# Optimization experiments

Hardware: AMD Instinct MI355X
Metric: run time of the kernel (lower is better)

The kernel has to match this reference:

```python
import jax, jax.numpy as jnp
import numpy as np

B, L, C = 8, 4096, 256  # batches, points per batch, channels
C8 = C // 8             # query/key projection dim


def setup_inputs() -> dict:
    key = jax.random.key(0)
    ks = jax.random.split(key, 8)
    feats = jax.random.normal(ks[0], (B * L, C), dtype=jnp.float32)
    s_in = 1.0 / np.sqrt(C)
    Wq = jax.random.normal(ks[1], (C8, C), dtype=jnp.float32) * s_in
    bq = jax.random.normal(ks[2], (C8,), dtype=jnp.float32) * 0.01
    Wk = jax.random.normal(ks[3], (C8, C), dtype=jnp.float32) * s_in
    bk = jax.random.normal(ks[4], (C8,), dtype=jnp.float32) * 0.01
    Wv = jax.random.normal(ks[5], (C, C), dtype=jnp.float32) * s_in
    bv = jax.random.normal(ks[6], (C,), dtype=jnp.float32) * 0.01
    # torch init is gamma=0 which zeroes the attention branch; use a nonzero
    # scalar so the attention path contributes to output/gradients.
    gamma = jnp.float32(0.5)
    return {"feats": feats, "Wq": Wq, "bq": bq, "Wk": Wk, "bk": bk,
            "Wv": Wv, "bv": bv, "gamma": gamma,
            "batch_size": B, "points_per_batch": L}


def reference(feats, Wq, bq, Wk, bk, Wv, bv, gamma, batch_size, points_per_batch):
    n, c = feats.shape
    x = feats.reshape(batch_size, points_per_batch, c)  # [B, L, C]
    # conv1d with kernel_size=1 == per-point linear projection
    q = jnp.einsum('blc,dc->bld', x, Wq) + bq  # [B, L, C8]
    k = jnp.einsum('blc,dc->bld', x, Wk) + bk  # [B, L, C8]
    v = jnp.einsum('blc,dc->bld', x, Wv) + bv  # [B, L, C]
    energy = jnp.einsum('bid,bjd->bij', q, k)  # unscaled scores [B, L, L]
    attn = jax.nn.softmax(energy, axis=-1)
    # torch: out[c, l] = sum_j V[c, j] * attn[l, j]  -> [B, C, L]
    out_cl = jnp.einsum('bjc,blj->bcl', v, attn)
    # faithful to torch .view(batch_size, C): raw reshape of [C, L] -> [L, C]
    out = out_cl.reshape(batch_size, points_per_batch, c)
    y = gamma * out + x
    return y.reshape(n, c)
```

## Files before the change

kernel.cpp:

```cpp
#include <hip/hip_runtime.h>

#define LOG2E 1.44269504088896340736f

typedef __attribute__((ext_vector_type(4)))  float  f32x4;
typedef __attribute__((ext_vector_type(16))) float  f32x16;
typedef __attribute__((ext_vector_type(8)))  __bf16 bf16x8;
typedef __attribute__((ext_vector_type(4)))  __bf16 bf16x4;

static __device__ __forceinline__ f32x4 mfma16(bf16x8 a, bf16x8 b, f32x4 c) {
  return __builtin_amdgcn_mfma_f32_16x16x32_bf16(a, b, c, 0, 0, 0);
}
static __device__ __forceinline__ f32x16 mfma32(bf16x8 a, bf16x8 b, f32x16 c) {
  return __builtin_amdgcn_mfma_f32_32x32x16_bf16(a, b, c, 0, 0, 0);
}


__global__ void cvt_f32_to_bf16(const float* __restrict__ s, __bf16* __restrict__ d, int n4) {
  const int stride = gridDim.x * blockDim.x;
  for (int i = blockIdx.x * blockDim.x + threadIdx.x; i < n4; i += stride) {
    const float4 v = reinterpret_cast<const float4*>(s)[i];
    bf16x4 o = { (__bf16)v.x, (__bf16)v.y, (__bf16)v.z, (__bf16)v.w };
    reinterpret_cast<bf16x4*>(d)[i] = o;
  }
}

__global__ __launch_bounds__(256) void cvt_weights(
    const float* __restrict__ wq, const float* __restrict__ wk, const float* __restrict__ wv,
    __bf16* __restrict__ dq, __bf16* __restrict__ dk, __bf16* __restrict__ dv) {
  const int i = blockIdx.x * 256 + threadIdx.x;
  const float* s; __bf16* d; int off;
  if (i < 2048)      { s = wq; d = dq; off = i; }
  else if (i < 4096) { s = wk; d = dk; off = i - 2048; }
  else               { s = wv; d = dv; off = i - 4096; }
  const float4 v = reinterpret_cast<const float4*>(s)[off];
  bf16x4 o = { (__bf16)v.x, (__bf16)v.y, (__bf16)v.z, (__bf16)v.w };
  reinterpret_cast<bf16x4*>(d)[off] = o;
}

__global__ __launch_bounds__(256) void qk_proj(
    const __bf16* __restrict__ x, const __bf16* __restrict__ wq, const __bf16* __restrict__ wk,
    const float* __restrict__ bq, const float* __restrict__ bk,
    __bf16* __restrict__ Qh, __bf16* __restrict__ Ql,
    __bf16* __restrict__ Kh, __bf16* __restrict__ Kl)
{
  const int w = threadIdx.x >> 6, lane = threadIdx.x & 63;
  const int lo = lane & 15, hi = lane >> 4;
  const int m0 = blockIdx.x * 64 + w * 16;
  f32x4 acc[4] = {};
  for (int ks = 0; ks < 8; ++ks) {
    const bf16x8 a = *reinterpret_cast<const bf16x8*>(x + (size_t)(m0 + lo) * 256 + ks * 32 + hi * 8);
    #pragma unroll
    for (int nt = 0; nt < 4; ++nt) {
      const int d = nt * 16 + lo;
      const __bf16* wrow = (nt < 2) ? (wq + d * 256) : (wk + (d - 32) * 256);
      const bf16x8 bfr = *reinterpret_cast<const bf16x8*>(wrow + ks * 32 + hi * 8);
      acc[nt] = mfma16(a, bfr, acc[nt]);
    }
  }
  #pragma unroll
  for (int nt = 0; nt < 4; ++nt) {
    const int d = nt * 16 + lo;
    const float bias = (nt < 2) ? bq[d] : bk[d - 32];
    #pragma unroll
    for (int r = 0; r < 4; ++r) {
      const size_t row = m0 + hi * 4 + r;
      float v = acc[nt][r] + bias;
      if (nt < 2) v *= LOG2E;
      const __bf16 vh = (__bf16)v;
      const __bf16 vl = (__bf16)(v - (float)vh);
      if (nt < 2) { Qh[row * 32 + d] = vh;        Ql[row * 32 + d] = vl; }
      else        { Kh[row * 32 + (d - 32)] = vh; Kl[row * 32 + (d - 32)] = vl; }
    }
  }
}

__global__ __launch_bounds__(256) void v_proj(
    const __bf16* __restrict__ x, const __bf16* __restrict__ wv, const float* __restrict__ bv,
    __bf16* __restrict__ VT)
{
  const int w = threadIdx.x >> 6, lane = threadIdx.x & 63;
  const int lo = lane & 15, hi = lane >> 4;
  const int bn = blockIdx.x & 511, bc = blockIdx.x >> 9;
  const int n0 = bn * 64;
  const int c0 = bc * 64 + w * 16;
  f32x4 acc[4] = {};
  for (int ks = 0; ks < 8; ++ks) {
    const bf16x8 a = *reinterpret_cast<const bf16x8*>(wv + (size_t)(c0 + lo) * 256 + ks * 32 + hi * 8);
    #pragma unroll
    for (int nt = 0; nt < 4; ++nt) {
      const bf16x8 bfr = *reinterpret_cast<const bf16x8*>(x + (size_t)(n0 + nt * 16 + lo) * 256 + ks * 32 + hi * 8);
      acc[nt] = mfma16(bfr, a, acc[nt]);
    }
  }
  const int bb = n0 >> 12;
  const int c = c0 + lo;
  const float bias = bv[c];
  #pragma unroll
  for (int nt = 0; nt < 4; ++nt) {
    const int n = (n0 + nt * 16 + hi * 4) & 4095;
    bf16x4 pk = { (__bf16)(acc[nt][0] + bias), (__bf16)(acc[nt][1] + bias),
                  (__bf16)(acc[nt][2] + bias), (__bf16)(acc[nt][3] + bias) };
    *reinterpret_cast<bf16x4*>(VT + (size_t)(bb * 256 + c) * 4096 + n) = pk;
  }
}

__global__ __launch_bounds__(512) void attn_kernel(
    const __bf16* __restrict__ Qhi, const __bf16* __restrict__ Qlo,
    const __bf16* __restrict__ Khi, const __bf16* __restrict__ Klo,
    const __bf16* __restrict__ VT,
    const float* __restrict__ feats, const float* __restrict__ gptr,
    float* __restrict__ out)
{
  __shared__ alignas(16) __bf16 vlds[2][8][1024];
  __shared__ alignas(16) __bf16 pbuf[2][4096];

  const int tid = threadIdx.x;
  const int w   = tid >> 6, lane = tid & 63;
  const int lo  = lane & 15, hi = lane >> 4;
  const int l31 = lane & 31, h  = lane >> 5;
  const int qt  = w & 3, jt = w >> 2;
  const int b    = blockIdx.x & 7;
  const int qblk = (blockIdx.x >> 3) * 64;

  const int qi = (b * 4096 + qblk + qt * 16 + lo) * 32 + hi * 8;
  const bf16x8 qh_ = *reinterpret_cast<const bf16x8*>(Qhi + qi);
  const bf16x8 ql_ = *reinterpret_cast<const bf16x8*>(Qlo + qi);

  const int kbase = (b * 4096 + jt * 16 + lo) * 32 + hi * 8;

  const __bf16* vsrc[2];
  #pragma unroll
  for (int g = 0; g < 2; ++g) {
    const int cl = g * 16 + (lane >> 2);
    const int sl = (lane & 3) ^ ((cl >> 1) & 3);
    vsrc[g] = VT + (size_t)(b * 256 + w * 32 + cl) * 4096 + sl * 8;
  }

  const int q    = qt * 16 + lo;
  const int swq  = (q ^ (q >> 3)) & 7;
  const int pwby = q * 128 + (((jt * 2 + (hi >> 1)) ^ swq) << 4) + ((hi & 1) << 3);
  int prow[2], swp[2];
  #pragma unroll
  for (int qg = 0; qg < 2; ++qg) {
    const int qq = qg * 32 + l31;
    prow[qg] = qq * 128;
    swp[qg]  = (qq ^ (qq >> 3)) & 7;
  }
  const int vswz = (l31 >> 1) & 3;

  f32x16 o0 = {}, o1 = {};
  f32x4  lacc = {};
  bf16x8 kh[2], kl[2];

  #define STAGE_V(JB, BUF)                                                        \
    { _Pragma("unroll")                                                           \
      for (int g = 0; g < 2; ++g) {                                               \
        __builtin_amdgcn_global_load_lds(                                         \
            (const __attribute__((address_space(1))) void*)(vsrc[g] + (JB)),      \
            (__attribute__((address_space(3))) void*)(&vlds[BUF][w][g * 512 + lane * 8]), \
            16, 0, 0);                                                            \
      } }

  #define QKSM(CUR)                                                               \
    { f32x4 s_ = {0.f, 0.f, 0.f, 0.f};                                            \
      s_ = mfma16(kh[CUR], qh_, s_);                                              \
      s_ = mfma16(kl[CUR], qh_, s_);                                              \
      s_ = mfma16(kh[CUR], ql_, s_);                                              \
      f32x4 p4;                                                                   \
      _Pragma("unroll")                                                           \
      for (int r = 0; r < 4; ++r) p4[r] = __builtin_amdgcn_exp2f(s_[r]);          \
      lacc += p4;                                                                 \
      bf16x4 pk = { (__bf16)p4[0], (__bf16)p4[1], (__bf16)p4[2], (__bf16)p4[3] }; \
      *reinterpret_cast<bf16x4*>((char*)&pbuf[CUR][0] + pwby) = pk; }

  #define PV_READS(PRV)                                                           \
    { const char* const pr = (const char*)&pbuf[PRV][0];                          \
      const char* const vr = (const char*)&vlds[PRV][w][0] + l31 * 64;            \
      _Pragma("unroll")                                                           \
      for (int ks = 0; ks < 2; ++ks) {                                            \
        pa0[ks] = *reinterpret_cast<const bf16x8*>(pr + prow[0] + ((((ks * 2 + h) ^ swp[0])) << 4)); \
        pa1[ks] = *reinterpret_cast<const bf16x8*>(pr + prow[1] + ((((ks * 2 + h) ^ swp[1])) << 4)); \
        vf[ks]  = *reinterpret_cast<const bf16x8*>(vr + ((((ks * 2 + h) ^ vswz)) << 4)); \
      } }

  #define PV_MFMA()                                                               \
    { __builtin_amdgcn_s_setprio(1);                                              \
      _Pragma("unroll")                                                           \
      for (int ks = 0; ks < 2; ++ks) {                                            \
        o0 = mfma32(pa0[ks], vf[ks], o0);                                         \
        o1 = mfma32(pa1[ks], vf[ks], o1);                                         \
      }                                                                           \
      __builtin_amdgcn_s_setprio(0); }

  kh[0] = *reinterpret_cast<const bf16x8*>(Khi + kbase);
  kl[0] = *reinterpret_cast<const bf16x8*>(Klo + kbase);
  STAGE_V(0, 0);
  __builtin_amdgcn_sched_barrier(0);

  {
    asm volatile("s_waitcnt vmcnt(2)" ::: "memory");
    __builtin_amdgcn_sched_barrier(0);
    QKSM(0)
    asm volatile("s_waitcnt lgkmcnt(0)" ::: "memory");
    __builtin_amdgcn_sched_barrier(0);
    kh[1] = *reinterpret_cast<const bf16x8*>(Khi + kbase + 1024);
    kl[1] = *reinterpret_cast<const bf16x8*>(Klo + kbase + 1024);
    STAGE_V(32, 1);
    __builtin_amdgcn_sched_barrier(0);
    __builtin_amdgcn_s_barrier();
    asm volatile("" ::: "memory");
  }

  #pragma unroll 2
  for (int t = 1; t < 128; ++t) {
    const int cur = t & 1, prv = cur ^ 1;
    const int jn  = ((t + 1) * 32) & 4095;

    asm volatile("s_waitcnt vmcnt(2)" ::: "memory");
    __builtin_amdgcn_sched_barrier(0);

    QKSM(cur)

    bf16x8 pa0[2], pa1[2], vf[2];
    PV_READS(prv)

    asm volatile("s_waitcnt lgkmcnt(0)" ::: "memory");
    __builtin_amdgcn_sched_barrier(0);

    kh[prv] = *reinterpret_cast<const bf16x8*>(Khi + kbase + jn * 32);
    kl[prv] = *reinterpret_cast<const bf16x8*>(Klo + kbase + jn * 32);
    STAGE_V(jn, prv);
    __builtin_amdgcn_sched_barrier(0);

    PV_MFMA()

    __builtin_amdgcn_s_barrier();
    asm volatile("" ::: "memory");
    __builtin_amdgcn_sched_barrier(0);
  }

  {
    asm volatile("s_waitcnt vmcnt(0)" ::: "memory");
    __builtin_amdgcn_sched_barrier(0);
    bf16x8 pa0[2], pa1[2], vf[2];
    PV_READS(1)
    PV_MFMA()
  }

  #undef STAGE_V
  #undef QKSM
  #undef PV_READS
  #undef PV_MFMA

  float la = lacc[0] + lacc[1] + lacc[2] + lacc[3];
  la += __shfl_xor(la, 16);
  la += __shfl_xor(la, 32);
  float* const lp = (float*)&pbuf[0][0];
  __syncthreads();
  if (lane < 16) lp[jt * 64 + qt * 16 + lo] = la;
  __syncthreads();

  const float g = gptr[0];
  const int c = w * 32 + l31;
  const size_t obase = (size_t)b * (256 * 4096) + (size_t)c * 4096 + qblk;
  #pragma unroll
  for (int qg = 0; qg < 2; ++qg) {
    const f32x16& o_ = qg ? o1 : o0;
    #pragma unroll
    for (int grp = 0; grp < 4; ++grp) {
      const int q0 = qg * 32 + grp * 8 + 4 * h;
      const f32x4 lv0 = *reinterpret_cast<const f32x4*>(&lp[q0]);
      const f32x4 lv1 = *reinterpret_cast<const f32x4*>(&lp[64 + q0]);
      const size_t idx = obase + q0;
      const float4 xr = *reinterpret_cast<const float4*>(feats + idx);
      float4 y;
      y.x = o_[grp * 4 + 0] * (g / (lv0[0] + lv1[0])) + xr.x;
      y.y = o_[grp * 4 + 1] * (g / (lv0[1] + lv1[1])) + xr.y;
      y.z = o_[grp * 4 + 2] * (g / (lv0[2] + lv1[2])) + xr.z;
      y.w = o_[grp * 4 + 3] * (g / (lv0[3] + lv1[3])) + xr.w;
      *reinterpret_cast<float4*>(out + idx) = y;
    }
  }
}

extern "C" void kernel_launch(void* const* d_in, const int* in_sizes, int n_in,
                              void* d_out, int out_size, void* d_ws, size_t ws_size,
                              hipStream_t stream) {
  const float* feats = (const float*)d_in[0];
  const float* Wq    = (const float*)d_in[1];
  const float* bq    = (const float*)d_in[2];
  const float* Wk    = (const float*)d_in[3];
  const float* bk    = (const float*)d_in[4];
  const float* Wv    = (const float*)d_in[5];
  const float* bv    = (const float*)d_in[6];
  const float* gamma = (const float*)d_in[7];
  float* out = (float*)d_out;

  char* ws = (char*)d_ws;
  const size_t SZ_X  = 16777216;
  const size_t SZ_QK = 2097152;
  const size_t SZ_VT = 16777216;
  const size_t NEED = SZ_X + 4 * SZ_QK + SZ_VT + 2 * 16384 + 131072;
  if (ws_size < NEED) return;

  __bf16* xb  = (__bf16*)(ws);
  __bf16* Qh  = (__bf16*)(ws + SZ_X);
  __bf16* Ql  = (__bf16*)(ws + SZ_X + SZ_QK);
  __bf16* Kh  = (__bf16*)(ws + SZ_X + 2 * SZ_QK);
  __bf16* Kl  = (__bf16*)(ws + SZ_X + 3 * SZ_QK);
  __bf16* VT  = (__bf16*)(ws + SZ_X + 4 * SZ_QK);
  __bf16* wqb = (__bf16*)(ws + SZ_X + 4 * SZ_QK + SZ_VT);
  __bf16* wkb = wqb + 32 * 256;
  __bf16* wvb = wkb + 32 * 256;

  cvt_f32_to_bf16<<<2048, 256, 0, stream>>>(feats, xb, 8388608 / 4);
  cvt_weights<<<80, 256, 0, stream>>>(Wq, Wk, Wv, wqb, wkb, wvb);

  qk_proj<<<512, 256, 0, stream>>>(xb, wqb, wkb, bq, bk, Qh, Ql, Kh, Kl);
  v_proj <<<2048, 256, 0, stream>>>(xb, wvb, bv, VT);
  attn_kernel<<<512, 512, 0, stream>>>(Qh, Ql, Kh, Kl, VT, feats, gamma, out);
}
```

Measured before the change: 191.8 us.

## Enlarge v_proj register tile, reswizzle V LDS layout, set attention occupancy hint

v_proj now has each block compute a 64-point by 256-channel tile, with each wave producing 4x4 MFMA sub-tiles. This reuses the x fragments across channels and cuts the grid from 2048 to 512 blocks, at the cost of more accumulator registers. The attention kernel's V staging into LDS switches to a 128-byte-row XOR swizzle so that the PV fragment reads avoid bank conflicts. A launch_bounds min-blocks hint of 2 is added to attn_kernel, which may constrain register allocation.

```diff
diff --git a/kernel.cpp b/kernel.cpp
--- a/kernel.cpp
+++ b/kernel.cpp
@@ -80,31 +80,38 @@
 {
   const int w = threadIdx.x >> 6, lane = threadIdx.x & 63;
   const int lo = lane & 15, hi = lane >> 4;
-  const int bn = blockIdx.x & 511, bc = blockIdx.x >> 9;
-  const int n0 = bn * 64;
-  const int c0 = bc * 64 + w * 16;
-  f32x4 acc[4] = {};
+  const int n0 = blockIdx.x * 64;
+  const int bb = n0 >> 12;
+  f32x4 acc[4][4] = {};
   for (int ks = 0; ks < 8; ++ks) {
-    const bf16x8 a = *reinterpret_cast<const bf16x8*>(wv + (size_t)(c0 + lo) * 256 + ks * 32 + hi * 8);
+    bf16x8 xa[4], wa[4];
+    #pragma unroll
+    for (int nt = 0; nt < 4; ++nt)
+      xa[nt] = *reinterpret_cast<const bf16x8*>(x + (size_t)(n0 + nt * 16 + lo) * 256 + ks * 32 + hi * 8);
+    #pragma unroll
+    for (int ct = 0; ct < 4; ++ct)
+      wa[ct] = *reinterpret_cast<const bf16x8*>(wv + (size_t)(w * 64 + ct * 16 + lo) * 256 + ks * 32 + hi * 8);
+    #pragma unroll
+    for (int nt = 0; nt < 4; ++nt)
+      #pragma unroll
+      for (int ct = 0; ct < 4; ++ct)
+        acc[nt][ct] = mfma16(xa[nt], wa[ct], acc[nt][ct]);
+  }
+  #pragma unroll
+  for (int ct = 0; ct < 4; ++ct) {
+    const int c = w * 64 + ct * 16 + lo;
+    const float bias = bv[c];
     #pragma unroll
     for (int nt = 0; nt < 4; ++nt) {
-      const bf16x8 bfr = *reinterpret_cast<const bf16x8*>(x + (size_t)(n0 + nt * 16 + lo) * 256 + ks * 32 + hi * 8);
-      acc[nt] = mfma16(bfr, a, acc[nt]);
+      const int n = (n0 + nt * 16 + hi * 4) & 4095;
+      bf16x4 pk = { (__bf16)(acc[nt][ct][0] + bias), (__bf16)(acc[nt][ct][1] + bias),
+                    (__bf16)(acc[nt][ct][2] + bias), (__bf16)(acc[nt][ct][3] + bias) };
+      *reinterpret_cast<bf16x4*>(VT + (size_t)(bb * 256 + c) * 4096 + n) = pk;
     }
   }
-  const int bb = n0 >> 12;
-  const int c = c0 + lo;
-  const float bias = bv[c];
-  #pragma unroll
-  for (int nt = 0; nt < 4; ++nt) {
-    const int n = (n0 + nt * 16 + hi * 4) & 4095;
-    bf16x4 pk = { (__bf16)(acc[nt][0] + bias), (__bf16)(acc[nt][1] + bias),
-                  (__bf16)(acc[nt][2] + bias), (__bf16)(acc[nt][3] + bias) };
-    *reinterpret_cast<bf16x4*>(VT + (size_t)(bb * 256 + c) * 4096 + n) = pk;
-  }
-}
-
-__global__ __launch_bounds__(512) void attn_kernel(
+}
+
+__global__ __launch_bounds__(512, 2) void attn_kernel(
     const __bf16* __restrict__ Qhi, const __bf16* __restrict__ Qlo,
     const __bf16* __restrict__ Khi, const __bf16* __restrict__ Klo,
     const __bf16* __restrict__ VT,
@@ -131,9 +138,10 @@
   const __bf16* vsrc[2];
   #pragma unroll
   for (int g = 0; g < 2; ++g) {
-    const int cl = g * 16 + (lane >> 2);
-    const int sl = (lane & 3) ^ ((cl >> 1) & 3);
-    vsrc[g] = VT + (size_t)(b * 256 + w * 32 + cl) * 4096 + sl * 8;
+    const int row = g * 8 + (lane >> 3);
+    const int lgc = (lane & 7) ^ (lane >> 3);
+    const int cl  = 2 * row + (lgc >> 2);
+    vsrc[g] = VT + (size_t)(b * 256 + w * 32 + cl) * 4096 + (lgc & 3) * 8;
   }
 
   const int q    = qt * 16 + lo;
@@ -146,7 +154,9 @@
     prow[qg] = qq * 128;
     swp[qg]  = (qq ^ (qq >> 3)) & 7;
   }
-  const int vswz = (l31 >> 1) & 3;
+  const int vrow = (l31 >> 1) * 128;
+  const int vlg  = (l31 & 1) * 4;
+  const int vxr  = (l31 >> 1) & 7;
 
   f32x16 o0 = {}, o1 = {};
   f32x4  lacc = {};
@@ -175,12 +185,12 @@
 
   #define PV_READS(PRV)                                                           \
     { const char* const pr = (const char*)&pbuf[PRV][0];                          \
-      const char* const vr = (const char*)&vlds[PRV][w][0] + l31 * 64;            \
+      const char* const vr = (const char*)&vlds[PRV][w][0] + vrow;                \
       _Pragma("unroll")                                                           \
       for (int ks = 0; ks < 2; ++ks) {                                            \
         pa0[ks] = *reinterpret_cast<const bf16x8*>(pr + prow[0] + ((((ks * 2 + h) ^ swp[0])) << 4)); \
         pa1[ks] = *reinterpret_cast<const bf16x8*>(pr + prow[1] + ((((ks * 2 + h) ^ swp[1])) << 4)); \
-        vf[ks]  = *reinterpret_cast<const bf16x8*>(vr + ((((ks * 2 + h) ^ vswz)) << 4)); \
+        vf[ks]  = *reinterpret_cast<const bf16x8*>(vr + ((((vlg + ks * 2 + h) ^ vxr)) << 4)); \
       } }
 
   #define PV_MFMA()                                                               \
@@ -317,6 +327,6 @@
   cvt_weights<<<80, 256, 0, stream>>>(Wq, Wk, Wv, wqb, wkb, wvb);
 
   qk_proj<<<512, 256, 0, stream>>>(xb, wqb, wkb, bq, bk, Qh, Ql, Kh, Kl);
-  v_proj <<<2048, 256, 0, stream>>>(xb, wvb, bv, VT);
+  v_proj <<<512, 256, 0, stream>>>(xb, wvb, bv, VT);
   attn_kernel<<<512, 512, 0, stream>>>(Qh, Ql, Kh, Kl, VT, feats, gamma, out);
 }
```

Result: faster. 170.0 us (-11.4%).
